# Kernel tuning notes

Hardware: AMD Instinct MI355X
Metric: run time of the kernel (lower is better)

The kernel has to match this reference:

```python
import jax, jax.numpy as jnp
import numpy as np

EPS = 1e-8
D = 1024      # embedding_dim
NH = 4        # num_heads
HD = D // NH  # head_dim
B, S = 4, 2048


def setup_inputs() -> dict:
    key = jax.random.key(0)
    k1, k2 = jax.random.split(key)
    x = jax.random.normal(k1, (B, S, 4 * D), dtype=jnp.float32)
    # small-init std = sqrt(2/(5*head_dim)) as in reset_parameters
    std = float(np.sqrt(2.0 / (5.0 * HD)))
    gate_weights = jax.random.normal(k2, (4, NH, HD, HD), dtype=jnp.float32) * std
    # biases: z,i,o zero; f gets powerlaw init (block 0 of 1 -> exponent 0.3)
    term = jnp.arange(HD, dtype=jnp.float32) / (HD - 1.0)
    f_bias = -(-5.0 + 12.0 * term ** 0.3)  # [HD]
    gate_biases = jnp.zeros((4, NH, HD), dtype=jnp.float32)
    gate_biases = gate_biases.at[2].set(jnp.broadcast_to(f_bias, (NH, HD)))
    return {"x_gate_inputs": x, "gate_weights": gate_weights, "gate_biases": gate_biases}


def _slstm_forward(x, W, biases):
    Bn, Sn, _ = x.shape
    # split into 4 gate pre-activations and apply headwise linear per gate
    xg = x.reshape(Bn, Sn, 4, NH, HD)           # gate order z,i,f,o along axis 2
    xg = jnp.moveaxis(xg, 2, 0)                  # [4,B,S,NH,HD]
    # headwise projection: einsum over head-in dim, per gate g and head h
    gates = jnp.einsum('gbshi,ghoi->gbsho', xg, W) + biases[:, None, None]  # [4,B,S,NH,HD]
    gates = jnp.moveaxis(gates, 2, 0)            # [S,4,B,NH,HD] for scan over time

    h0 = jnp.zeros((Bn, NH, HD), dtype=x.dtype)
    carry0 = (h0, h0, h0, jnp.zeros((Bn, NH, HD), dtype=jnp.float32))

    def step(carry, g_t):
        h, c, n, m = carry
        z_b, i_b, f_b, o_b = g_t[0], g_t[1], g_t[2], g_t[3]
        z_val = jnp.tanh(z_b)
        o_val = jax.nn.sigmoid(o_b)
        # faithful to original: exp then log(.+EPS), in m-state dtype (fp32)
        log_f = jnp.log(jnp.exp(f_b).astype(jnp.float32) + EPS)
        log_i = jnp.log(jnp.exp(i_b).astype(jnp.float32) + EPS)
        m_new = jnp.maximum(log_f + m, log_i)
        i_hat = jnp.exp(log_i - m_new).astype(x.dtype)
        f_hat = jnp.exp(log_f + m - m_new).astype(x.dtype)
        c_new = f_hat * c + i_hat * z_val
        n_new = f_hat * n + i_hat
        h_new = o_val * (c_new / (n_new + EPS))
        return (h_new, c_new, n_new, m_new), h_new

    (h_f, c_f, n_f, m_f), hs = jax.lax.scan(step, carry0, gates)
    h_seq = jnp.moveaxis(hs, 0, 1)               # [B,S,NH,HD]
    return h_seq, (h_f, c_f, n_f, m_f)


def reference(x_gate_inputs, gate_weights, gate_biases):
    h_seq, (h_f, c_f, n_f, m_f) = _slstm_forward(x_gate_inputs, gate_weights, gate_biases)
    return h_seq, h_f, c_f, n_f, m_f
```

## Files before the change

### kernel.cpp

```cpp
#include <hip/hip_runtime.h>
#include <cstdint>

#define S_LEN   2048
#define BATCH   4
#define NCH     4096
#define PLANE   ((size_t)S_LEN * NCH)
#define CHUNK   32
#define NCHUNK  64
#define SN      ((size_t)NCHUNK * NCH)
#define EPS     1e-8f

using bf16x8 = __attribute__((ext_vector_type(8))) short;
using f32x4  = __attribute__((ext_vector_type(4))) float;
typedef unsigned short u16;

__device__ __forceinline__ short f2bf(float f) {
  uint32_t u = __builtin_bit_cast(uint32_t, f);
  u += 0x7fffu + ((u >> 16) & 1u);
  return (short)(u >> 16);
}
__device__ __forceinline__ float bf2f(u16 u) {
  return __builtin_bit_cast(float, (uint32_t)u << 16);
}

__global__ __launch_bounds__(1024) void gates_gemm3(
    const float* __restrict__ x, const float* __restrict__ W,
    const float* __restrict__ bias,
    u16* __restrict__ gz16, float* __restrict__ gi, float* __restrict__ gf,
    u16* __restrict__ go16) {
  __shared__ u16 As[2][16 * 264];

  const int gh  = blockIdx.x;
  const int rg  = blockIdx.y;
  const int g   = gh >> 2, hh = gh & 3;
  const int tid = threadIdx.x;
  const int wave = tid >> 6, lane = tid & 63;
  const int l16 = lane & 15, quad = lane >> 4;
  const int n0  = wave * 16;
  const int row0 = rg * 256;

  bf16x8 Bf[8];
  {
    const float* wp = W + ((size_t)gh << 16) + (n0 + l16) * 256 + quad * 8;
#pragma unroll
    for (int kt = 0; kt < 8; ++kt) {
      float4 w0 = *(const float4*)(wp + kt * 32);
      float4 w1 = *(const float4*)(wp + kt * 32 + 4);
      bf16x8 b;
      b[0] = f2bf(w0.x); b[1] = f2bf(w0.y); b[2] = f2bf(w0.z); b[3] = f2bf(w0.w);
      b[4] = f2bf(w1.x); b[5] = f2bf(w1.y); b[6] = f2bf(w1.z); b[7] = f2bf(w1.w);
      Bf[kt] = b;
    }
  }
  const float bv = bias[gh * 256 + n0 + l16];

  const int sr = tid >> 6, sc = tid & 63;
  const float* sbase = x + (size_t)(row0 + sr) * 4096 + g * 1024 + hh * 256 + sc * 4;

  float4 sreg;
  auto gload = [&](int t) { sreg = *(const float4*)(sbase + (size_t)t * 16 * 4096); };
  auto swrite = [&](int buf) {
    ushort4 u;
    u.x = (u16)f2bf(sreg.x); u.y = (u16)f2bf(sreg.y);
    u.z = (u16)f2bf(sreg.z); u.w = (u16)f2bf(sreg.w);
    *(ushort4*)&As[buf][sr * 264 + sc * 4] = u;
  };

  gload(0); swrite(0);
  __syncthreads();

  for (int t = 0; t < 16; ++t) {
    if (t + 1 < 16) gload(t + 1);

    f32x4 acc = (f32x4){0.f, 0.f, 0.f, 0.f};
#pragma unroll
    for (int kt = 0; kt < 8; ++kt) {
      bf16x8 a = *(const bf16x8*)&As[t & 1][l16 * 264 + kt * 32 + quad * 8];
      acc = __builtin_amdgcn_mfma_f32_16x16x32_bf16(a, Bf[kt], acc, 0, 0, 0);
    }

#pragma unroll
    for (int rr = 0; rr < 4; ++rr) {
      int rowi = row0 + t * 16 + quad * 4 + rr;
      int sx = rowi & (S_LEN - 1);
      int bx = rowi >> 11;
      size_t idx = (size_t)sx * NCH + bx * 1024 + hh * 256 + n0 + l16;
      float v = acc[rr] + bv;
      if (g == 1)      gi[idx] = v;
      else if (g == 2) gf[idx] = v;
      else if (g == 0) {
        float tz = 1.f - 2.f * __builtin_amdgcn_rcpf(1.f + __expf(2.f * v));
        gz16[idx] = (u16)f2bf(tz);
      } else {
        float s = __builtin_amdgcn_rcpf(1.f + __expf(-v));
        go16[idx] = (u16)f2bf(s);
      }
    }

    if (t + 1 < 16) {
      swrite((t + 1) & 1);
      __syncthreads();
    }
  }
}

__global__ __launch_bounds__(256) void scan_pass1(
    const u16* __restrict__ gz16, const float* __restrict__ gi,
    const float* __restrict__ gf, float* __restrict__ sums) {
  const int t  = blockIdx.x * 256 + threadIdx.x;
  const int ch = t & (NCH - 1);
  const int ck = t >> 12;
  const size_t base = (size_t)ck * CHUNK * NCH + ch;

  float A = 0.f, Bv = -1e30f, D = 0.f, Dn = 0.f;

  float z0[8], i0[8], f0[8], z1[8], i1[8], f1[8];
#pragma unroll
  for (int j = 0; j < 8; ++j) {
    size_t off = base + (size_t)j * NCH;
    z0[j] = bf2f(gz16[off]); i0[j] = gi[off]; f0[j] = gf[off];
  }

  auto step = [&](float z, float i, float f) {
    float Bn = fmaxf(Bv + f, i);
    float e1 = __expf(Bv + f - Bn);
    float e2 = __expf(i - Bn);
    D  = e1 * D + e2 * z;
    Dn = e1 * Dn + e2;
    A += f;
    Bv = Bn;
  };

  for (int gb = 0; gb < 4; gb += 2) {
#pragma unroll
    for (int j = 0; j < 8; ++j) {
      size_t off = base + (size_t)((gb + 1) * 8 + j) * NCH;
      z1[j] = bf2f(gz16[off]); i1[j] = gi[off]; f1[j] = gf[off];
    }
#pragma unroll
    for (int j = 0; j < 8; ++j) step(z0[j], i0[j], f0[j]);
    if (gb + 2 < 4) {
#pragma unroll
      for (int j = 0; j < 8; ++j) {
        size_t off = base + (size_t)((gb + 2) * 8 + j) * NCH;
        z0[j] = bf2f(gz16[off]); i0[j] = gi[off]; f0[j] = gf[off];
      }
    }
#pragma unroll
    for (int j = 0; j < 8; ++j) step(z1[j], i1[j], f1[j]);
  }

  const size_t idx = (size_t)ck * NCH + ch;
  sums[idx]          = A;
  sums[SN + idx]     = Bv;
  sums[2 * SN + idx] = D;
  sums[3 * SN + idx] = Dn;
}

__global__ __launch_bounds__(256) void scan_pass2(
    const float* __restrict__ sums, float* __restrict__ ent) {
  const int ch = blockIdx.x * 256 + threadIdx.x;
  float c = 0.f, n = 0.f, m = 0.f;

  float A0 = sums[ch], B0 = sums[SN + ch], D0 = sums[2 * SN + ch], N0 = sums[3 * SN + ch];
  for (int k = 0; k < NCHUNK; ++k) {
    float A1 = 0.f, B1 = 0.f, D1 = 0.f, N1 = 0.f;
    if (k + 1 < NCHUNK) {
      size_t ni = (size_t)(k + 1) * NCH + ch;
      A1 = sums[ni]; B1 = sums[SN + ni]; D1 = sums[2 * SN + ni]; N1 = sums[3 * SN + ni];
    }
    size_t idx = (size_t)k * NCH + ch;
    ent[idx]          = c;
    ent[SN + idx]     = n;
    ent[2 * SN + idx] = m;
    float mo = fmaxf(m + A0, B0);
    float ea = __expf(m + A0 - mo);
    float eb = __expf(B0 - mo);
    c = ea * c + eb * D0;
    n = ea * n + eb * N0;
    m = mo;
    A0 = A1; B0 = B1; D0 = D1; N0 = N1;
  }
}

__global__ __launch_bounds__(256) void scan_pass3(
    const u16* __restrict__ gz16, const float* __restrict__ gi,
    const float* __restrict__ gf, const u16* __restrict__ go16,
    const float* __restrict__ ent, float* __restrict__ out) {
  const int t  = blockIdx.x * 256 + threadIdx.x;
  const int ch = t & (NCH - 1);
  const int ck = t >> 12;

  const size_t idx0 = (size_t)ck * NCH + ch;
  float c = ent[idx0];
  float n = ent[SN + idx0];
  float m = ent[2 * SN + idx0];

  const int b = ch >> 10, d = ch & 1023;
  const size_t base = (size_t)ck * CHUNK * NCH + ch;
  float* hout = out + (size_t)b * (S_LEN * 1024) + (size_t)(ck * CHUNK) * 1024 + d;

  float hv = 0.f;
  float z0[8], i0[8], f0[8], o0[8], z1[8], i1[8], f1[8], o1[8];
#pragma unroll
  for (int j = 0; j < 8; ++j) {
    size_t off = base + (size_t)j * NCH;
    z0[j] = bf2f(gz16[off]); i0[j] = gi[off]; f0[j] = gf[off]; o0[j] = bf2f(go16[off]);
  }

  auto step = [&](float z, float i, float f, float o, int s) {
    float mn = fmaxf(f + m, i);
    float fh = __expf(f + m - mn);
    float ih = __expf(i - mn);
    c = fh * c + ih * z;
    n = fh * n + ih;
    m = mn;
    hv = o * c * __builtin_amdgcn_rcpf(n + EPS);
    hout[(size_t)s * 1024] = hv;
  };

  for (int gb = 0; gb < 4; gb += 2) {
#pragma unroll
    for (int j = 0; j < 8; ++j) {
      size_t off = base + (size_t)((gb + 1) * 8 + j) * NCH;
      z1[j] = bf2f(gz16[off]); i1[j] = gi[off]; f1[j] = gf[off]; o1[j] = bf2f(go16[off]);
    }
#pragma unroll
    for (int j = 0; j < 8; ++j) step(z0[j], i0[j], f0[j], o0[j], gb * 8 + j);
    if (gb + 2 < 4) {
#pragma unroll
      for (int j = 0; j < 8; ++j) {
        size_t off = base + (size_t)((gb + 2) * 8 + j) * NCH;
        z0[j] = bf2f(gz16[off]); i0[j] = gi[off]; f0[j] = gf[off]; o0[j] = bf2f(go16[off]);
      }
    }
#pragma unroll
    for (int j = 0; j < 8; ++j) step(z1[j], i1[j], f1[j], o1[j], (gb + 1) * 8 + j);
  }

  if (ck == NCHUNK - 1) {
    float* fin = out + (size_t)BATCH * S_LEN * 1024;
    fin[ch]            = hv;
    fin[NCH + ch]      = c;
    fin[2 * NCH + ch]  = n;
    fin[3 * NCH + ch]  = m;
  }
}

extern "C" void kernel_launch(void* const* d_in, const int* in_sizes, int n_in,
                              void* d_out, int out_size, void* d_ws, size_t ws_size,
                              hipStream_t stream) {
  const float* x    = (const float*)d_in[0];
  const float* W    = (const float*)d_in[1];
  const float* bias = (const float*)d_in[2];
  float* out = (float*)d_out;

  u16*   gz16 = (u16*)d_ws;
  float* gi   = (float*)(gz16 + PLANE);
  float* gf   = gi + PLANE;
  u16*   go16 = (u16*)(gf + PLANE);
  float* sums = (float*)(go16 + PLANE);
  float* ent  = sums + 4 * SN;

  gates_gemm3<<<dim3(16, 32), dim3(1024), 0, stream>>>(x, W, bias, gz16, gi, gf, go16);
  scan_pass1<<<dim3(1024), dim3(256), 0, stream>>>(gz16, gi, gf, sums);
  scan_pass2<<<dim3(16), dim3(256), 0, stream>>>(sums, ent);
  scan_pass3<<<dim3(1024), dim3(256), 0, stream>>>(gz16, gi, gf, go16, ent, out);
}
```

Baseline: 277.9 us.

## Parallelize chunk-carry scan across wave lanes and deepen prefetch in GEMM and scans

The serial 64-step per-channel carry combine in pass2 becomes a wave-level Hillis-Steele shuffle scan, with one lane per chunk and many more blocks. The gates GEMM now prefetches two tiles ahead, defers all epilogue stores until after the MFMA loop, pads the LDS row stride, and uses a lighter barrier. Scan passes 1 and 3 switch to triple-buffered register prefetch and get occupancy hints. The parallel combine reorders the log-space arithmetic, which may shift rounding slightly, and the deferred GEMM stores keep 16 accumulator vectors live, which raises register pressure.

```diff
diff --git a/kernel.cpp b/kernel.cpp
--- a/kernel.cpp
+++ b/kernel.cpp
@@ -22,13 +22,16 @@
 __device__ __forceinline__ float bf2f(u16 u) {
   return __builtin_bit_cast(float, (uint32_t)u << 16);
 }
-
-__global__ __launch_bounds__(1024) void gates_gemm3(
+__device__ __forceinline__ void lds_barrier() {
+  asm volatile("s_waitcnt lgkmcnt(0)\n\ts_barrier" ::: "memory");
+}
+
+__global__ __launch_bounds__(1024) void gates_gemm4(
     const float* __restrict__ x, const float* __restrict__ W,
     const float* __restrict__ bias,
     u16* __restrict__ gz16, float* __restrict__ gi, float* __restrict__ gf,
     u16* __restrict__ go16) {
-  __shared__ u16 As[2][16 * 264];
+  __shared__ u16 As[2][16 * 272];
 
   const int gh  = blockIdx.x;
   const int rg  = blockIdx.y;
@@ -57,35 +60,48 @@
   const int sr = tid >> 6, sc = tid & 63;
   const float* sbase = x + (size_t)(row0 + sr) * 4096 + g * 1024 + hh * 256 + sc * 4;
 
-  float4 sreg;
-  auto gload = [&](int t) { sreg = *(const float4*)(sbase + (size_t)t * 16 * 4096); };
-  auto swrite = [&](int buf) {
+  auto swrite = [&](int buf, float4 v) {
     ushort4 u;
-    u.x = (u16)f2bf(sreg.x); u.y = (u16)f2bf(sreg.y);
-    u.z = (u16)f2bf(sreg.z); u.w = (u16)f2bf(sreg.w);
-    *(ushort4*)&As[buf][sr * 264 + sc * 4] = u;
+    u.x = (u16)f2bf(v.x); u.y = (u16)f2bf(v.y);
+    u.z = (u16)f2bf(v.z); u.w = (u16)f2bf(v.w);
+    *(ushort4*)&As[buf][sr * 272 + sc * 4] = u;
   };
 
-  gload(0); swrite(0);
-  __syncthreads();
-
+  float4 pf[2];
+  pf[0] = *(const float4*)(sbase);
+  pf[1] = *(const float4*)(sbase + (size_t)16 * 4096);
+  swrite(0, pf[0]);
+  lds_barrier();
+
+  f32x4 acc[16];
+#pragma unroll
+  for (int t = 0; t < 16; ++t) acc[t] = (f32x4){0.f, 0.f, 0.f, 0.f};
+
+#pragma unroll
   for (int t = 0; t < 16; ++t) {
-    if (t + 1 < 16) gload(t + 1);
-
-    f32x4 acc = (f32x4){0.f, 0.f, 0.f, 0.f};
+    if (t + 2 < 16) pf[t & 1] = *(const float4*)(sbase + (size_t)(t + 2) * 16 * 4096);
+
 #pragma unroll
     for (int kt = 0; kt < 8; ++kt) {
-      bf16x8 a = *(const bf16x8*)&As[t & 1][l16 * 264 + kt * 32 + quad * 8];
-      acc = __builtin_amdgcn_mfma_f32_16x16x32_bf16(a, Bf[kt], acc, 0, 0, 0);
-    }
-
+      bf16x8 a = *(const bf16x8*)&As[t & 1][l16 * 272 + kt * 32 + quad * 8];
+      acc[t] = __builtin_amdgcn_mfma_f32_16x16x32_bf16(a, Bf[kt], acc[t], 0, 0, 0);
+    }
+
+    if (t + 1 < 16) {
+      swrite((t + 1) & 1, pf[(t + 1) & 1]);
+      lds_barrier();
+    }
+  }
+
+#pragma unroll
+  for (int t = 0; t < 16; ++t) {
 #pragma unroll
     for (int rr = 0; rr < 4; ++rr) {
       int rowi = row0 + t * 16 + quad * 4 + rr;
       int sx = rowi & (S_LEN - 1);
       int bx = rowi >> 11;
       size_t idx = (size_t)sx * NCH + bx * 1024 + hh * 256 + n0 + l16;
-      float v = acc[rr] + bv;
+      float v = acc[t][rr] + bv;
       if (g == 1)      gi[idx] = v;
       else if (g == 2) gf[idx] = v;
       else if (g == 0) {
@@ -96,15 +112,10 @@
         go16[idx] = (u16)f2bf(s);
       }
     }
-
-    if (t + 1 < 16) {
-      swrite((t + 1) & 1);
-      __syncthreads();
-    }
-  }
-}
-
-__global__ __launch_bounds__(256) void scan_pass1(
+  }
+}
+
+__global__ __launch_bounds__(256, 4) void scan_pass1(
     const u16* __restrict__ gz16, const float* __restrict__ gi,
     const float* __restrict__ gf, float* __restrict__ sums) {
   const int t  = blockIdx.x * 256 + threadIdx.x;
@@ -114,40 +125,34 @@
 
   float A = 0.f, Bv = -1e30f, D = 0.f, Dn = 0.f;
 
-  float z0[8], i0[8], f0[8], z1[8], i1[8], f1[8];
-#pragma unroll
-  for (int j = 0; j < 8; ++j) {
-    size_t off = base + (size_t)j * NCH;
-    z0[j] = bf2f(gz16[off]); i0[j] = gi[off]; f0[j] = gf[off];
-  }
-
-  auto step = [&](float z, float i, float f) {
-    float Bn = fmaxf(Bv + f, i);
-    float e1 = __expf(Bv + f - Bn);
-    float e2 = __expf(i - Bn);
-    D  = e1 * D + e2 * z;
-    Dn = e1 * Dn + e2;
-    A += f;
-    Bv = Bn;
+  u16 zb[3][8]; float ib[3][8], fb[3][8];
+
+  auto loadg = [&](int buf, int grp) {
+#pragma unroll
+    for (int j = 0; j < 8; ++j) {
+      size_t off = base + (size_t)(grp * 8 + j) * NCH;
+      zb[buf][j] = gz16[off]; ib[buf][j] = gi[off]; fb[buf][j] = gf[off];
+    }
   };
 
-  for (int gb = 0; gb < 4; gb += 2) {
-#pragma unroll
-    for (int j = 0; j < 8; ++j) {
-      size_t off = base + (size_t)((gb + 1) * 8 + j) * NCH;
-      z1[j] = bf2f(gz16[off]); i1[j] = gi[off]; f1[j] = gf[off];
-    }
-#pragma unroll
-    for (int j = 0; j < 8; ++j) step(z0[j], i0[j], f0[j]);
-    if (gb + 2 < 4) {
-#pragma unroll
-      for (int j = 0; j < 8; ++j) {
-        size_t off = base + (size_t)((gb + 2) * 8 + j) * NCH;
-        z0[j] = bf2f(gz16[off]); i0[j] = gi[off]; f0[j] = gf[off];
-      }
-    }
-#pragma unroll
-    for (int j = 0; j < 8; ++j) step(z1[j], i1[j], f1[j]);
+  loadg(0, 0);
+  loadg(1, 1);
+
+#pragma unroll
+  for (int grp = 0; grp < 4; ++grp) {
+    if (grp + 2 < 4) loadg((grp + 2) % 3, grp + 2);
+    const int b = grp % 3;
+#pragma unroll
+    for (int j = 0; j < 8; ++j) {
+      float z = bf2f(zb[b][j]), i = ib[b][j], f = fb[b][j];
+      float Bn = fmaxf(Bv + f, i);
+      float e1 = __expf(Bv + f - Bn);
+      float e2 = __expf(i - Bn);
+      D  = e1 * D + e2 * z;
+      Dn = e1 * Dn + e2;
+      A += f;
+      Bv = Bn;
+    }
   }
 
   const size_t idx = (size_t)ck * NCH + ch;
@@ -159,31 +164,43 @@
 
 __global__ __launch_bounds__(256) void scan_pass2(
     const float* __restrict__ sums, float* __restrict__ ent) {
-  const int ch = blockIdx.x * 256 + threadIdx.x;
-  float c = 0.f, n = 0.f, m = 0.f;
-
-  float A0 = sums[ch], B0 = sums[SN + ch], D0 = sums[2 * SN + ch], N0 = sums[3 * SN + ch];
-  for (int k = 0; k < NCHUNK; ++k) {
-    float A1 = 0.f, B1 = 0.f, D1 = 0.f, N1 = 0.f;
-    if (k + 1 < NCHUNK) {
-      size_t ni = (size_t)(k + 1) * NCH + ch;
-      A1 = sums[ni]; B1 = sums[SN + ni]; D1 = sums[2 * SN + ni]; N1 = sums[3 * SN + ni];
-    }
-    size_t idx = (size_t)k * NCH + ch;
-    ent[idx]          = c;
-    ent[SN + idx]     = n;
-    ent[2 * SN + idx] = m;
-    float mo = fmaxf(m + A0, B0);
-    float ea = __expf(m + A0 - mo);
-    float eb = __expf(B0 - mo);
-    c = ea * c + eb * D0;
-    n = ea * n + eb * N0;
-    m = mo;
-    A0 = A1; B0 = B1; D0 = D1; N0 = N1;
-  }
-}
-
-__global__ __launch_bounds__(256) void scan_pass3(
+  const int gt   = blockIdx.x * 256 + threadIdx.x;
+  const int ch   = gt >> 6;
+  const int lane = threadIdx.x & 63;
+
+  const size_t idx = (size_t)lane * NCH + ch;
+  float A = sums[idx], B = sums[SN + idx];
+  float D = sums[2 * SN + idx], N = sums[3 * SN + idx];
+
+#pragma unroll
+  for (int d = 1; d < 64; d <<= 1) {
+    float A1 = __shfl_up(A, d, 64);
+    float B1 = __shfl_up(B, d, 64);
+    float D1 = __shfl_up(D, d, 64);
+    float N1 = __shfl_up(N, d, 64);
+    if (lane >= d) {
+      float Bn = fmaxf(B1 + A, B);
+      float s1 = __expf(B1 + A - Bn);
+      float s2 = __expf(B - Bn);
+      D = s1 * D1 + s2 * D;
+      N = s1 * N1 + s2 * N;
+      B = Bn;
+      A = A1 + A;
+    }
+  }
+
+  float Ax = __shfl_up(A, 1, 64), Bx = __shfl_up(B, 1, 64);
+  float Dx = __shfl_up(D, 1, 64), Nx = __shfl_up(N, 1, 64);
+  if (lane == 0) { Ax = 0.f; Bx = -1e30f; Dx = 0.f; Nx = 0.f; }
+
+  float mE = fmaxf(Ax, Bx);
+  float sc = __expf(Bx - mE);
+  ent[idx]          = sc * Dx;
+  ent[SN + idx]     = sc * Nx;
+  ent[2 * SN + idx] = mE;
+}
+
+__global__ __launch_bounds__(256, 4) void scan_pass3(
     const u16* __restrict__ gz16, const float* __restrict__ gi,
     const float* __restrict__ gf, const u16* __restrict__ go16,
     const float* __restrict__ ent, float* __restrict__ out) {
@@ -200,42 +217,37 @@
   const size_t base = (size_t)ck * CHUNK * NCH + ch;
   float* hout = out + (size_t)b * (S_LEN * 1024) + (size_t)(ck * CHUNK) * 1024 + d;
 
+  u16 zb[3][8], ob[3][8]; float ib[3][8], fb[3][8];
+
+  auto loadg = [&](int buf, int grp) {
+#pragma unroll
+    for (int j = 0; j < 8; ++j) {
+      size_t off = base + (size_t)(grp * 8 + j) * NCH;
+      zb[buf][j] = gz16[off]; ib[buf][j] = gi[off];
+      fb[buf][j] = gf[off];   ob[buf][j] = go16[off];
+    }
+  };
+
+  loadg(0, 0);
+  loadg(1, 1);
+
   float hv = 0.f;
-  float z0[8], i0[8], f0[8], o0[8], z1[8], i1[8], f1[8], o1[8];
-#pragma unroll
-  for (int j = 0; j < 8; ++j) {
-    size_t off = base + (size_t)j * NCH;
-    z0[j] = bf2f(gz16[off]); i0[j] = gi[off]; f0[j] = gf[off]; o0[j] = bf2f(go16[off]);
-  }
-
-  auto step = [&](float z, float i, float f, float o, int s) {
-    float mn = fmaxf(f + m, i);
-    float fh = __expf(f + m - mn);
-    float ih = __expf(i - mn);
-    c = fh * c + ih * z;
-    n = fh * n + ih;
-    m = mn;
-    hv = o * c * __builtin_amdgcn_rcpf(n + EPS);
-    hout[(size_t)s * 1024] = hv;
-  };
-
-  for (int gb = 0; gb < 4; gb += 2) {
-#pragma unroll
-    for (int j = 0; j < 8; ++j) {
-      size_t off = base + (size_t)((gb + 1) * 8 + j) * NCH;
-      z1[j] = bf2f(gz16[off]); i1[j] = gi[off]; f1[j] = gf[off]; o1[j] = bf2f(go16[off]);
-    }
-#pragma unroll
-    for (int j = 0; j < 8; ++j) step(z0[j], i0[j], f0[j], o0[j], gb * 8 + j);
-    if (gb + 2 < 4) {
-#pragma unroll
-      for (int j = 0; j < 8; ++j) {
-        size_t off = base + (size_t)((gb + 2) * 8 + j) * NCH;
-        z0[j] = bf2f(gz16[off]); i0[j] = gi[off]; f0[j] = gf[off]; o0[j] = bf2f(go16[off]);
-      }
-    }
-#pragma unroll
-    for (int j = 0; j < 8; ++j) step(z1[j], i1[j], f1[j], o1[j], (gb + 1) * 8 + j);
+#pragma unroll
+  for (int grp = 0; grp < 4; ++grp) {
+    if (grp + 2 < 4) loadg((grp + 2) % 3, grp + 2);
+    const int bu = grp % 3;
+#pragma unroll
+    for (int j = 0; j < 8; ++j) {
+      float z = bf2f(zb[bu][j]), i = ib[bu][j], f = fb[bu][j], o = bf2f(ob[bu][j]);
+      float mn = fmaxf(f + m, i);
+      float fh = __expf(f + m - mn);
+      float ih = __expf(i - mn);
+      c = fh * c + ih * z;
+      n = fh * n + ih;
+      m = mn;
+      hv = o * c * __builtin_amdgcn_rcpf(n + EPS);
+      hout[(size_t)(grp * 8 + j) * 1024] = hv;
+    }
   }
 
   if (ck == NCHUNK - 1) {
@@ -262,8 +274,8 @@
   float* sums = (float*)(go16 + PLANE);
   float* ent  = sums + 4 * SN;
 
-  gates_gemm3<<<dim3(16, 32), dim3(1024), 0, stream>>>(x, W, bias, gz16, gi, gf, go16);
+  gates_gemm4<<<dim3(16, 32), dim3(1024), 0, stream>>>(x, W, bias, gz16, gi, gf, go16);
   scan_pass1<<<dim3(1024), dim3(256), 0, stream>>>(gz16, gi, gf, sums);
-  scan_pass2<<<dim3(16), dim3(256), 0, stream>>>(sums, ent);
+  scan_pass2<<<dim3(1024), dim3(256), 0, stream>>>(sums, ent);
   scan_pass3<<<dim3(1024), dim3(256), 0, stream>>>(gz16, gi, gf, go16, ent, out);
 }
```

Measured after the change: 279.5 us. About the same (+0.6%).
